# Performance work log

Hardware: AMD Instinct MI355X
Metric: run time of the kernel (lower is better)

The kernel has to match this reference:

```python
import jax, jax.numpy as jnp
import numpy as np

N, D, H = 4096, 128, 8


def setup_inputs() -> dict:
    key = jax.random.key(0)
    ks = jax.random.split(key, 9)
    s = 1.0 / np.sqrt(D)
    return {
        "x": jax.random.normal(ks[0], (N, D), jnp.float32),
        "Wq": jax.random.normal(ks[1], (H, D, D), jnp.float32) * s,
        "bq": jax.random.normal(ks[2], (H, D), jnp.float32) * s,
        "Wk": jax.random.normal(ks[3], (H, D, D), jnp.float32) * s,
        "bk": jax.random.normal(ks[4], (H, D), jnp.float32) * s,
        "Wv": jax.random.normal(ks[5], (H, D, D), jnp.float32) * s,
        "bv": jax.random.normal(ks[6], (H, D), jnp.float32) * s,
        "Wo": jax.random.normal(ks[7], (H * D, D), jnp.float32) * s,
        "bo": jax.random.normal(ks[8], (D,), jnp.float32) * s,
    }


def reference(x, Wq, bq, Wk, bk, Wv, bv, Wo, bo):
    # Batched per-head projections: [H, N, D]
    q = jnp.einsum('nd,hde->hne', x, Wq) + bq[:, None, :]
    k = jnp.einsum('nd,hde->hne', x, Wk) + bk[:, None, :]
    v = jnp.einsum('nd,hde->hne', x, Wv) + bv[:, None, :]
    # Non-standard attention: scores = v @ q.T  -> [H, N, N]
    scores = jnp.einsum('hnd,hmd->hnm', v, q)
    wts = jax.nn.softmax(scores, axis=-1)
    out = jnp.einsum('hnm,hmd->hnd', wts, k)  # [H, N, D]
    # Concat heads along feature dim (head-major order, as torch.cat)
    outs = out.transpose(1, 0, 2).reshape(N, H * D)
    return outs @ Wo + bo
```

## Files before the change

### kernel.cpp

```cpp
#include <hip/hip_runtime.h>
#include <hip/hip_bf16.h>


typedef __attribute__((ext_vector_type(8))) short short8;
typedef __attribute__((ext_vector_type(4))) float f32x4;

#define MFMA(a,b,c) __builtin_amdgcn_mfma_f32_16x16x32_bf16((a),(b),(c),0,0,0)
#define LOG2E 1.44269504088896340736f
#define DEFER_THR 8.0f

#define AS1 __attribute__((address_space(1)))
#define AS3 __attribute__((address_space(3)))
static __device__ __forceinline__ void gld16(const void* g, void* l) {
  __builtin_amdgcn_global_load_lds((const AS1 void*)g, (AS3 void*)l, 16, 0, 0);
}

static __device__ __forceinline__ unsigned short f2bf(float f) {
  union { float f; unsigned u; } v; v.f = f;
  unsigned r = v.u + 0x7fffu + ((v.u >> 16) & 1u);
  return (unsigned short)(r >> 16);
}
static __device__ __forceinline__ float bf2f(unsigned short h) {
  union { unsigned u; float f; } v; v.u = ((unsigned)h) << 16; return v.f;
}
static __device__ __forceinline__ void split2(float f, unsigned short& hi, unsigned short& lo) {
  hi = f2bf(f);
  lo = f2bf(f - bf2f(hi));
}

__global__ __launch_bounds__(256) void kxbf(const float* __restrict__ x,
                                            unsigned short* __restrict__ xh,
                                            unsigned short* __restrict__ xl) {
  int i = blockIdx.x * 256 + threadIdx.x;
  float4 v = reinterpret_cast<const float4*>(x)[i];
  ushort4 oh, ol;
  split2(v.x, oh.x, ol.x); split2(v.y, oh.y, ol.y);
  split2(v.z, oh.z, ol.z); split2(v.w, oh.w, ol.w);
  reinterpret_cast<ushort4*>(xh)[i] = oh;
  reinterpret_cast<ushort4*>(xl)[i] = ol;
}

__global__ __launch_bounds__(256) void kwt(const float* __restrict__ Wq,
                                           const float* __restrict__ Wk,
                                           const float* __restrict__ Wv,
                                           const float* __restrict__ Wo,
                                           unsigned short* __restrict__ WTh,
                                           unsigned short* __restrict__ WTl,
                                           unsigned short* __restrict__ WoT) {
  __shared__ float lds[64 * 130];
  int b = blockIdx.x, t = threadIdx.x;
  const float* src; int isWo;
  if (b < 24) {
    int slot = b >> 3, hh = b & 7;
    src = (slot == 0 ? Wq : (slot == 1 ? Wk : Wv)) + hh * 16384;
    isWo = 0;
  } else {
    src = Wo + (b - 24) * 16384;
    isWo = 1;
  }
  for (int half = 0; half < 2; ++half) {
#pragma unroll
    for (int i = 0; i < 8; ++i) {
      int lin = i * 1024 + t * 4;
      int row = lin >> 7, col = lin & 127;
      float4 v = *reinterpret_cast<const float4*>(src + half * 8192 + lin);
      lds[row * 130 + col + 0] = v.x;
      lds[row * 130 + col + 1] = v.y;
      lds[row * 130 + col + 2] = v.z;
      lds[row * 130 + col + 3] = v.w;
    }
    __syncthreads();
    int e = t >> 1, k0 = (t & 1) * 32;
    float buf[32];
#pragma unroll
    for (int j = 0; j < 32; ++j) buf[j] = lds[(k0 + j) * 130 + e];
    int kg = half * 64 + k0;
    if (!isWo) {
      unsigned short* dh = WTh + b * 16384 + e * 128 + kg;
      unsigned short* dl = WTl + b * 16384 + e * 128 + kg;
#pragma unroll
      for (int c = 0; c < 4; ++c) {
        short8 oh, ol;
#pragma unroll
        for (int jj = 0; jj < 8; ++jj) {
          unsigned short h, l; split2(buf[c * 8 + jj], h, l);
          oh[jj] = (short)h; ol[jj] = (short)l;
        }
        *reinterpret_cast<short8*>(dh + c * 8) = oh;
        *reinterpret_cast<short8*>(dl + c * 8) = ol;
      }
    } else {
      unsigned short* dst = WoT + e * 1024 + (b - 24) * 128 + kg;
#pragma unroll
      for (int c = 0; c < 4; ++c) {
        short8 o;
#pragma unroll
        for (int jj = 0; jj < 8; ++jj) o[jj] = (short)f2bf(buf[c * 8 + jj]);
        *reinterpret_cast<short8*>(dst + c * 8) = o;
      }
    }
    __syncthreads();
  }
}

__global__ __launch_bounds__(256) void kproj(const unsigned short* __restrict__ xh,
                                             const unsigned short* __restrict__ xl,
                                             const unsigned short* __restrict__ WThg,
                                             const unsigned short* __restrict__ WTlg,
                                             const float* __restrict__ bq,
                                             const float* __restrict__ bk,
                                             const float* __restrict__ bv,
                                             unsigned short* __restrict__ Qh,
                                             unsigned short* __restrict__ Vh,
                                             unsigned short* __restrict__ Vl,
                                             unsigned short* __restrict__ Kt) {
  __shared__ __align__(16) unsigned char lds[64 * 128 * 2];
  int nb = blockIdx.x, h = blockIdx.y, z = blockIdx.z;
  int t = threadIdx.x, lane = t & 63, w = t >> 6;
  int r = lane & 15, g = lane >> 4;
  int slot = (z == 0) ? 0 : (z == 1 ? 2 : 1);
  const unsigned short* Wth = WThg + (slot * 8 + h) * 16384;
  const unsigned short* Wtl = WTlg + (slot * 8 + h) * 16384;
  const float* bias = (z == 0) ? bq : (z == 1 ? bv : bk);
  int rowbase = nb * 64 + w * 16;

  short8 ah[4], al[4];
#pragma unroll
  for (int kc = 0; kc < 4; ++kc) {
    ah[kc] = *reinterpret_cast<const short8*>(xh + (rowbase + r) * 128 + kc * 32 + g * 8);
    al[kc] = *reinterpret_cast<const short8*>(xl + (rowbase + r) * 128 + kc * 32 + g * 8);
  }
  f32x4 acc[8];
#pragma unroll
  for (int ct = 0; ct < 8; ++ct) acc[ct] = (f32x4){0.f, 0.f, 0.f, 0.f};
  if (z < 2) {
#pragma unroll
    for (int ct = 0; ct < 8; ++ct) {
#pragma unroll
      for (int kc = 0; kc < 4; ++kc) {
        short8 bh = *reinterpret_cast<const short8*>(Wth + (ct * 16 + r) * 128 + kc * 32 + g * 8);
        short8 bl = *reinterpret_cast<const short8*>(Wtl + (ct * 16 + r) * 128 + kc * 32 + g * 8);
        acc[ct] = MFMA(ah[kc], bh, acc[ct]);
        acc[ct] = MFMA(ah[kc], bl, acc[ct]);
        acc[ct] = MFMA(al[kc], bh, acc[ct]);
      }
    }
    unsigned short* dh = ((z == 0) ? Qh : Vh) + (size_t)h * 4096 * 128;
    unsigned short* dl = Vl + (size_t)h * 4096 * 128;
#pragma unroll
    for (int ct = 0; ct < 8; ++ct) {
      int e = ct * 16 + r;
      float bb = bias[h * 128 + e];
#pragma unroll
      for (int rr = 0; rr < 4; ++rr) {
        int n = rowbase + g * 4 + rr;
        float fv = acc[ct][rr] + bb;
        if (z == 0) {
          dh[n * 128 + e] = f2bf(fv);
        } else {
          unsigned short hi_, lo_; split2(fv, hi_, lo_);
          dh[n * 128 + e] = hi_;
          dl[n * 128 + e] = lo_;
        }
      }
    }
  } else {
#pragma unroll
    for (int ct = 0; ct < 8; ++ct) {
#pragma unroll
      for (int kc = 0; kc < 4; ++kc) {
        short8 bh = *reinterpret_cast<const short8*>(Wth + (ct * 16 + r) * 128 + kc * 32 + g * 8);
        acc[ct] = MFMA(ah[kc], bh, acc[ct]);
      }
    }
#pragma unroll
    for (int ct = 0; ct < 8; ++ct) {
      int e = ct * 16 + r;
      float bb = bias[h * 128 + e];
#pragma unroll
      for (int rr = 0; rr < 4; ++rr) {
        int n = w * 16 + g * 4 + rr;
        unsigned off = ((unsigned)(n * 128 + e) * 2u) ^ ((unsigned)(n & 7) << 4);
        *reinterpret_cast<unsigned short*>(lds + off) = f2bf(acc[ct][rr] + bb);
      }
    }
    __syncthreads();
    int e = t >> 1, n0 = (t & 1) * 32;
    unsigned short buf[32];
#pragma unroll
    for (int j = 0; j < 32; ++j) {
      int n = n0 + j;
      unsigned off = ((unsigned)(n * 128 + e) * 2u) ^ ((unsigned)(n & 7) << 4);
      buf[j] = *reinterpret_cast<unsigned short*>(lds + off);
    }
    unsigned short* dst = Kt + ((size_t)h * 128 + e) * 4096 + nb * 64 + n0;
#pragma unroll
    for (int c = 0; c < 4; ++c) {
      short8 o;
#pragma unroll
      for (int jj = 0; jj < 8; ++jj) o[jj] = (short)buf[c * 8 + jj];
      *reinterpret_cast<short8*>(dst + c * 8) = o;
    }
  }
}

__global__ __launch_bounds__(256, 4) void kattn(
    const unsigned short* __restrict__ Qg,
    const unsigned short* __restrict__ Kt,
    const unsigned short* __restrict__ Vh,
    const unsigned short* __restrict__ Vl,
    unsigned short* __restrict__ Opart,
    float2* __restrict__ ml) {
  __shared__ __align__(16) unsigned char qlds[2][8192];
  __shared__ __align__(16) unsigned char klds[2][8192];
  __shared__ __align__(16) unsigned short plds[4][16 * 40];
  const int h = blockIdx.x, nb = blockIdx.y, z = blockIdx.z;
  const int t = threadIdx.x, lane = t & 63, w = t >> 6;
  const int r = lane & 15, g = lane >> 4;
  const unsigned char* Qb = (const unsigned char*)(Qg + (size_t)h * 4096 * 128);
  const unsigned char* Kb = (const unsigned char*)(Kt + (size_t)h * 128 * 4096);

  const int qrow = t >> 4;
  const unsigned qcb = (unsigned)((t & 15) * 16);
  const int krow = t >> 2;
  const unsigned kmb = (unsigned)((t & 3) * 16);

  const int vrow = nb * 64 + w * 16 + r;
  short8 vah[4], val[4];
#pragma unroll
  for (int kc = 0; kc < 4; ++kc) {
    vah[kc] = *reinterpret_cast<const short8*>(Vh + (size_t)h * 4096 * 128 + (size_t)vrow * 128 + kc * 32 + g * 8);
    val[kc] = *reinterpret_cast<const short8*>(Vl + (size_t)h * 4096 * 128 + (size_t)vrow * 128 + kc * 32 + g * 8);
  }

  f32x4 oacc[8];
#pragma unroll
  for (int dt = 0; dt < 8; ++dt) oacc[dt] = (f32x4){0.f, 0.f, 0.f, 0.f};
  float mrun = -3e38f, lrun = 0.f;
  const int mt0 = z * 64;

#define STAGE(buf, mtile) do {                                                   \
    const size_t mQ = (size_t)(mtile) * 32 * 256;                                \
    const size_t mK = (size_t)(mtile) * 32 * 2;                                  \
    _Pragma("unroll")                                                            \
    for (int j = 0; j < 2; ++j) {                                                \
      int row = qrow + j * 16;                                                   \
      gld16(Qb + mQ + (size_t)row * 256 + (qcb ^ ((unsigned)(row & 7) << 4)),    \
            &qlds[buf][j * 4096 + t * 16]);                                      \
    }                                                                            \
    _Pragma("unroll")                                                            \
    for (int j = 0; j < 2; ++j) {                                                \
      int d = krow + j * 64;                                                     \
      gld16(Kb + (size_t)d * 8192 + mK + kmb,                                    \
            &klds[buf][j * 4096 + t * 16]);                                      \
    }                                                                            \
  } while (0)

  STAGE(0, mt0);
  __syncthreads();

  const unsigned qsw = ((unsigned)(r & 7)) << 4;
  for (int it = 0; it < 64; ++it) {
    const int buf = it & 1;
    if (it < 63) STAGE(buf ^ 1, mt0 + it + 1);
    f32x4 s0 = (f32x4){0.f, 0.f, 0.f, 0.f};
    f32x4 s1 = (f32x4){0.f, 0.f, 0.f, 0.f};
    __builtin_amdgcn_s_setprio(1);
#pragma unroll
    for (int kc = 0; kc < 4; ++kc) {
      unsigned col = (unsigned)(kc * 64 + g * 16);
      short8 q0 = *reinterpret_cast<const short8*>(&qlds[buf][(unsigned)r * 256 + (col ^ qsw)]);
      short8 q1 = *reinterpret_cast<const short8*>(&qlds[buf][(unsigned)(16 + r) * 256 + (col ^ qsw)]);
      s0 = MFMA(q0, vah[kc], s0);
      s1 = MFMA(q1, vah[kc], s1);
      s0 = MFMA(q0, val[kc], s0);
      s1 = MFMA(q1, val[kc], s1);
    }
    __builtin_amdgcn_s_setprio(0);
    float mx = fmaxf(fmaxf(fmaxf(s0[0], s0[1]), fmaxf(s0[2], s0[3])),
                     fmaxf(fmaxf(s1[0], s1[1]), fmaxf(s1[2], s1[3])));
    mx = fmaxf(mx, __shfl_xor(mx, 16));
    mx = fmaxf(mx, __shfl_xor(mx, 32));
    if (__any(mx > mrun + DEFER_THR)) {
      float nm = fmaxf(mrun, mx);
      float sc = exp2f((mrun - nm) * LOG2E);
      lrun *= sc;
#pragma unroll
      for (int dt = 0; dt < 8; ++dt) oacc[dt] *= sc;
      mrun = nm;
    }
    float p[8];
#pragma unroll
    for (int j = 0; j < 4; ++j) {
      p[j]     = exp2f((s0[j] - mrun) * LOG2E);
      p[4 + j] = exp2f((s1[j] - mrun) * LOG2E);
    }
    float ps = ((p[0] + p[1]) + (p[2] + p[3])) + ((p[4] + p[5]) + (p[6] + p[7]));
    ps += __shfl_xor(ps, 16);
    ps += __shfl_xor(ps, 32);
    lrun += ps;
    ushort4 pk0, pk1;
    pk0.x = f2bf(p[0]); pk0.y = f2bf(p[1]); pk0.z = f2bf(p[2]); pk0.w = f2bf(p[3]);
    pk1.x = f2bf(p[4]); pk1.y = f2bf(p[5]); pk1.z = f2bf(p[6]); pk1.w = f2bf(p[7]);
    unsigned short* pw = &plds[w][r * 40];
    *reinterpret_cast<ushort4*>(pw + g * 4)      = pk0;
    *reinterpret_cast<ushort4*>(pw + 16 + g * 4) = pk1;
    short8 pa = *reinterpret_cast<const short8*>(&plds[w][r * 40 + g * 8]);
    __builtin_amdgcn_s_setprio(1);
#pragma unroll
    for (int dt = 0; dt < 8; ++dt) {
      short8 kb = *reinterpret_cast<const short8*>(&klds[buf][(unsigned)(dt * 16 + r) * 64 + (unsigned)(g * 16)]);
      oacc[dt] = MFMA(kb, pa, oacc[dt]);
    }
    __builtin_amdgcn_s_setprio(0);
    __syncthreads();
  }
#undef STAGE
  unsigned short* Ob = Opart + ((size_t)(z * 8 + h) * 4096 + vrow) * 128;
#pragma unroll
  for (int dt = 0; dt < 8; ++dt) {
    ushort4 o4;
    o4.x = f2bf(oacc[dt][0]); o4.y = f2bf(oacc[dt][1]);
    o4.z = f2bf(oacc[dt][2]); o4.w = f2bf(oacc[dt][3]);
    *reinterpret_cast<ushort4*>(Ob + dt * 16 + g * 4) = o4;
  }
  if (g == 0) ml[(size_t)(z * 8 + h) * 4096 + vrow] = make_float2(mrun, lrun);
}

__global__ __launch_bounds__(256) void kmerge(const unsigned short* __restrict__ Opart,
                                              const float2* __restrict__ ml,
                                              unsigned short* __restrict__ OUTS) {
  int tid = blockIdx.x * 256 + threadIdx.x;
  int q = tid & 31, n = (tid >> 5) & 4095, h = tid >> 17;
  float2 ml0 = ml[(size_t)h * 4096 + n];
  float2 ml1 = ml[(size_t)(8 + h) * 4096 + n];
  float M = fmaxf(ml0.x, ml1.x);
  float a0 = exp2f((ml0.x - M) * LOG2E);
  float a1 = exp2f((ml1.x - M) * LOG2E);
  float inv = 1.0f / (ml0.y * a0 + ml1.y * a1);
  a0 *= inv; a1 *= inv;
  ushort4 o0 = *reinterpret_cast<const ushort4*>(Opart + ((size_t)h * 4096 + n) * 128 + q * 4);
  ushort4 o1 = *reinterpret_cast<const ushort4*>(Opart + ((size_t)(8 + h) * 4096 + n) * 128 + q * 4);
  ushort4 o;
  o.x = f2bf(bf2f(o0.x) * a0 + bf2f(o1.x) * a1);
  o.y = f2bf(bf2f(o0.y) * a0 + bf2f(o1.y) * a1);
  o.z = f2bf(bf2f(o0.z) * a0 + bf2f(o1.z) * a1);
  o.w = f2bf(bf2f(o0.w) * a0 + bf2f(o1.w) * a1);
  *reinterpret_cast<ushort4*>(OUTS + (size_t)n * 1024 + h * 128 + q * 4) = o;
}

__global__ __launch_bounds__(256) void kout(const unsigned short* __restrict__ OUTS,
                                            const unsigned short* __restrict__ WoT,
                                            const float* __restrict__ bo,
                                            float* __restrict__ out) {
  int rb = blockIdx.x, ch = blockIdx.y;
  int t = threadIdx.x, lane = t & 63, w = t >> 6;
  int r = lane & 15, g = lane >> 4;
  int row = rb * 16 + r;
  int e0 = ch * 64 + w * 16;
  f32x4 acc = (f32x4){0.f, 0.f, 0.f, 0.f};
#pragma unroll
  for (int kc = 0; kc < 32; ++kc) {
    short8 a = *reinterpret_cast<const short8*>(OUTS + (size_t)row * 1024 + kc * 32 + g * 8);
    short8 b = *reinterpret_cast<const short8*>(WoT + (size_t)(e0 + r) * 1024 + kc * 32 + g * 8);
    acc = MFMA(a, b, acc);
  }
  float bov = bo[e0 + r];
#pragma unroll
  for (int rr = 0; rr < 4; ++rr) {
    int n = rb * 16 + g * 4 + rr;
    out[(size_t)n * 128 + e0 + r] = acc[rr] + bov;
  }
}

extern "C" void kernel_launch(void* const* d_in, const int* in_sizes, int n_in,
                              void* d_out, int out_size, void* d_ws, size_t ws_size,
                              hipStream_t stream) {
  const float* x  = (const float*)d_in[0];
  const float* Wq = (const float*)d_in[1];
  const float* bq = (const float*)d_in[2];
  const float* Wk = (const float*)d_in[3];
  const float* bk = (const float*)d_in[4];
  const float* Wv = (const float*)d_in[5];
  const float* bv = (const float*)d_in[6];
  const float* Wo = (const float*)d_in[7];
  const float* bo = (const float*)d_in[8];
  float* out = (float*)d_out;

  unsigned short* ws = (unsigned short*)d_ws;
  unsigned short* xh    = ws;
  unsigned short* xl    = xh + 524288;
  unsigned short* WTh   = xl + 524288;
  unsigned short* WTl   = WTh + 393216;
  unsigned short* WoT   = WTl + 393216;
  unsigned short* Qh    = WoT + 131072;
  unsigned short* Vh    = Qh + 4194304;
  unsigned short* Vl    = Vh + 4194304;
  unsigned short* Kt    = Vl + 4194304;
  unsigned short* OUTS  = Kt + 4194304;
  unsigned short* Opart = OUTS + 4194304;
  float2*         mlp   = (float2*)(Opart + 8388608);

  kxbf<<<512, 256, 0, stream>>>(x, xh, xl);
  kwt<<<32, 256, 0, stream>>>(Wq, Wk, Wv, Wo, WTh, WTl, WoT);
  kproj<<<dim3(64, 8, 3), 256, 0, stream>>>(xh, xl, WTh, WTl, bq, bk, bv,
                                            Qh, Vh, Vl, Kt);
  kattn<<<dim3(8, 64, 2), 256, 0, stream>>>(Qh, Kt, Vh, Vl, Opart, mlp);
  kmerge<<<4096, 256, 0, stream>>>(Opart, mlp, OUTS);
  kout<<<dim3(256, 2), 256, 0, stream>>>(OUTS, WoT, bo, out);
}
```

Before: 285.4 us.

## Fuse x conversion into projection, widen attention tiles, fuse merge into output GEMM

Drops the separate x bf16-split kernel and splits x inside the projection kernel, which now computes Q, V and K in one block per row tile instead of three z-slices. The attention kernel moves to 128-thread blocks in which each wave handles 32 V rows, so every staged Q/K tile is reused across twice as many rows. The split-softmax merge is folded into the output projection, which also computes all 128 output columns per block. This removes two launches and the OUTS intermediate, at the cost of more registers in the attention kernel and scalar (non-vector) Opart stores.

After: 275.4 us. 3.5% less time.

```diff
diff --git a/kernel.cpp b/kernel.cpp
--- a/kernel.cpp
+++ b/kernel.cpp
@@ -26,18 +26,6 @@
 static __device__ __forceinline__ void split2(float f, unsigned short& hi, unsigned short& lo) {
   hi = f2bf(f);
   lo = f2bf(f - bf2f(hi));
-}
-
-__global__ __launch_bounds__(256) void kxbf(const float* __restrict__ x,
-                                            unsigned short* __restrict__ xh,
-                                            unsigned short* __restrict__ xl) {
-  int i = blockIdx.x * 256 + threadIdx.x;
-  float4 v = reinterpret_cast<const float4*>(x)[i];
-  ushort4 oh, ol;
-  split2(v.x, oh.x, ol.x); split2(v.y, oh.y, ol.y);
-  split2(v.z, oh.z, ol.z); split2(v.w, oh.w, ol.w);
-  reinterpret_cast<ushort4*>(xh)[i] = oh;
-  reinterpret_cast<ushort4*>(xl)[i] = ol;
 }
 
 __global__ __launch_bounds__(256) void kwt(const float* __restrict__ Wq,
@@ -103,37 +91,45 @@
   }
 }
 
-__global__ __launch_bounds__(256) void kproj(const unsigned short* __restrict__ xh,
-                                             const unsigned short* __restrict__ xl,
-                                             const unsigned short* __restrict__ WThg,
-                                             const unsigned short* __restrict__ WTlg,
-                                             const float* __restrict__ bq,
-                                             const float* __restrict__ bk,
-                                             const float* __restrict__ bv,
-                                             unsigned short* __restrict__ Qh,
-                                             unsigned short* __restrict__ Vh,
-                                             unsigned short* __restrict__ Vl,
-                                             unsigned short* __restrict__ Kt) {
+__global__ __launch_bounds__(256) void kprojf(const float* __restrict__ x,
+                                              const unsigned short* __restrict__ WThg,
+                                              const unsigned short* __restrict__ WTlg,
+                                              const float* __restrict__ bq,
+                                              const float* __restrict__ bk,
+                                              const float* __restrict__ bv,
+                                              unsigned short* __restrict__ Qh,
+                                              unsigned short* __restrict__ Vh,
+                                              unsigned short* __restrict__ Vl,
+                                              unsigned short* __restrict__ Kt) {
   __shared__ __align__(16) unsigned char lds[64 * 128 * 2];
-  int nb = blockIdx.x, h = blockIdx.y, z = blockIdx.z;
+  int nb = blockIdx.x, h = blockIdx.y;
   int t = threadIdx.x, lane = t & 63, w = t >> 6;
   int r = lane & 15, g = lane >> 4;
-  int slot = (z == 0) ? 0 : (z == 1 ? 2 : 1);
-  const unsigned short* Wth = WThg + (slot * 8 + h) * 16384;
-  const unsigned short* Wtl = WTlg + (slot * 8 + h) * 16384;
-  const float* bias = (z == 0) ? bq : (z == 1 ? bv : bk);
   int rowbase = nb * 64 + w * 16;
 
   short8 ah[4], al[4];
 #pragma unroll
   for (int kc = 0; kc < 4; ++kc) {
-    ah[kc] = *reinterpret_cast<const short8*>(xh + (rowbase + r) * 128 + kc * 32 + g * 8);
-    al[kc] = *reinterpret_cast<const short8*>(xl + (rowbase + r) * 128 + kc * 32 + g * 8);
-  }
+    const float* xp = x + (size_t)(rowbase + r) * 128 + kc * 32 + g * 8;
+    float4 f0 = *reinterpret_cast<const float4*>(xp);
+    float4 f1 = *reinterpret_cast<const float4*>(xp + 4);
+    unsigned short hi_, lo_;
+    split2(f0.x, hi_, lo_); ah[kc][0] = (short)hi_; al[kc][0] = (short)lo_;
+    split2(f0.y, hi_, lo_); ah[kc][1] = (short)hi_; al[kc][1] = (short)lo_;
+    split2(f0.z, hi_, lo_); ah[kc][2] = (short)hi_; al[kc][2] = (short)lo_;
+    split2(f0.w, hi_, lo_); ah[kc][3] = (short)hi_; al[kc][3] = (short)lo_;
+    split2(f1.x, hi_, lo_); ah[kc][4] = (short)hi_; al[kc][4] = (short)lo_;
+    split2(f1.y, hi_, lo_); ah[kc][5] = (short)hi_; al[kc][5] = (short)lo_;
+    split2(f1.z, hi_, lo_); ah[kc][6] = (short)hi_; al[kc][6] = (short)lo_;
+    split2(f1.w, hi_, lo_); ah[kc][7] = (short)hi_; al[kc][7] = (short)lo_;
+  }
+
   f32x4 acc[8];
-#pragma unroll
-  for (int ct = 0; ct < 8; ++ct) acc[ct] = (f32x4){0.f, 0.f, 0.f, 0.f};
-  if (z < 2) {
+  {
+    const unsigned short* Wth = WThg + (0 * 8 + h) * 16384;
+    const unsigned short* Wtl = WTlg + (0 * 8 + h) * 16384;
+#pragma unroll
+    for (int ct = 0; ct < 8; ++ct) acc[ct] = (f32x4){0.f, 0.f, 0.f, 0.f};
 #pragma unroll
     for (int ct = 0; ct < 8; ++ct) {
 #pragma unroll
@@ -145,26 +141,53 @@
         acc[ct] = MFMA(al[kc], bh, acc[ct]);
       }
     }
-    unsigned short* dh = ((z == 0) ? Qh : Vh) + (size_t)h * 4096 * 128;
-    unsigned short* dl = Vl + (size_t)h * 4096 * 128;
+    unsigned short* dh = Qh + (size_t)h * 4096 * 128;
 #pragma unroll
     for (int ct = 0; ct < 8; ++ct) {
       int e = ct * 16 + r;
-      float bb = bias[h * 128 + e];
+      float bb = bq[h * 128 + e];
 #pragma unroll
       for (int rr = 0; rr < 4; ++rr) {
         int n = rowbase + g * 4 + rr;
-        float fv = acc[ct][rr] + bb;
-        if (z == 0) {
-          dh[n * 128 + e] = f2bf(fv);
-        } else {
-          unsigned short hi_, lo_; split2(fv, hi_, lo_);
-          dh[n * 128 + e] = hi_;
-          dl[n * 128 + e] = lo_;
-        }
-      }
-    }
-  } else {
+        dh[n * 128 + e] = f2bf(acc[ct][rr] + bb);
+      }
+    }
+  }
+  {
+    const unsigned short* Wth = WThg + (2 * 8 + h) * 16384;
+    const unsigned short* Wtl = WTlg + (2 * 8 + h) * 16384;
+#pragma unroll
+    for (int ct = 0; ct < 8; ++ct) acc[ct] = (f32x4){0.f, 0.f, 0.f, 0.f};
+#pragma unroll
+    for (int ct = 0; ct < 8; ++ct) {
+#pragma unroll
+      for (int kc = 0; kc < 4; ++kc) {
+        short8 bh = *reinterpret_cast<const short8*>(Wth + (ct * 16 + r) * 128 + kc * 32 + g * 8);
+        short8 bl = *reinterpret_cast<const short8*>(Wtl + (ct * 16 + r) * 128 + kc * 32 + g * 8);
+        acc[ct] = MFMA(ah[kc], bh, acc[ct]);
+        acc[ct] = MFMA(ah[kc], bl, acc[ct]);
+        acc[ct] = MFMA(al[kc], bh, acc[ct]);
+      }
+    }
+    unsigned short* dh = Vh + (size_t)h * 4096 * 128;
+    unsigned short* dl = Vl + (size_t)h * 4096 * 128;
+#pragma unroll
+    for (int ct = 0; ct < 8; ++ct) {
+      int e = ct * 16 + r;
+      float bb = bv[h * 128 + e];
+#pragma unroll
+      for (int rr = 0; rr < 4; ++rr) {
+        int n = rowbase + g * 4 + rr;
+        unsigned short hi_, lo_; split2(acc[ct][rr] + bb, hi_, lo_);
+        dh[n * 128 + e] = hi_;
+        dl[n * 128 + e] = lo_;
+      }
+    }
+  }
+  {
+    const unsigned short* Wth = WThg + (1 * 8 + h) * 16384;
+#pragma unroll
+    for (int ct = 0; ct < 8; ++ct) acc[ct] = (f32x4){0.f, 0.f, 0.f, 0.f};
 #pragma unroll
     for (int ct = 0; ct < 8; ++ct) {
 #pragma unroll
@@ -176,7 +199,7 @@
 #pragma unroll
     for (int ct = 0; ct < 8; ++ct) {
       int e = ct * 16 + r;
-      float bb = bias[h * 128 + e];
+      float bb = bk[h * 128 + e];
 #pragma unroll
       for (int rr = 0; rr < 4; ++rr) {
         int n = w * 16 + g * 4 + rr;
@@ -204,7 +227,7 @@
   }
 }
 
-__global__ __launch_bounds__(256, 4) void kattn(
+__global__ __launch_bounds__(128, 2) void kattn(
     const unsigned short* __restrict__ Qg,
     const unsigned short* __restrict__ Kt,
     const unsigned short* __restrict__ Vh,
@@ -213,46 +236,48 @@
     float2* __restrict__ ml) {
   __shared__ __align__(16) unsigned char qlds[2][8192];
   __shared__ __align__(16) unsigned char klds[2][8192];
-  __shared__ __align__(16) unsigned short plds[4][16 * 40];
+  __shared__ __align__(16) unsigned short plds[2][32 * 40];
   const int h = blockIdx.x, nb = blockIdx.y, z = blockIdx.z;
   const int t = threadIdx.x, lane = t & 63, w = t >> 6;
   const int r = lane & 15, g = lane >> 4;
   const unsigned char* Qb = (const unsigned char*)(Qg + (size_t)h * 4096 * 128);
   const unsigned char* Kb = (const unsigned char*)(Kt + (size_t)h * 128 * 4096);
 
-  const int qrow = t >> 4;
-  const unsigned qcb = (unsigned)((t & 15) * 16);
-  const int krow = t >> 2;
-  const unsigned kmb = (unsigned)((t & 3) * 16);
-
-  const int vrow = nb * 64 + w * 16 + r;
-  short8 vah[4], val[4];
+  const int vbase = nb * 64 + w * 32;
+  short8 va0h[4], va0l[4], va1h[4], va1l[4];
 #pragma unroll
   for (int kc = 0; kc < 4; ++kc) {
-    vah[kc] = *reinterpret_cast<const short8*>(Vh + (size_t)h * 4096 * 128 + (size_t)vrow * 128 + kc * 32 + g * 8);
-    val[kc] = *reinterpret_cast<const short8*>(Vl + (size_t)h * 4096 * 128 + (size_t)vrow * 128 + kc * 32 + g * 8);
-  }
-
-  f32x4 oacc[8];
-#pragma unroll
-  for (int dt = 0; dt < 8; ++dt) oacc[dt] = (f32x4){0.f, 0.f, 0.f, 0.f};
-  float mrun = -3e38f, lrun = 0.f;
+    size_t o0 = (size_t)h * 4096 * 128 + (size_t)(vbase + r) * 128 + kc * 32 + g * 8;
+    size_t o1 = (size_t)h * 4096 * 128 + (size_t)(vbase + 16 + r) * 128 + kc * 32 + g * 8;
+    va0h[kc] = *reinterpret_cast<const short8*>(Vh + o0);
+    va0l[kc] = *reinterpret_cast<const short8*>(Vl + o0);
+    va1h[kc] = *reinterpret_cast<const short8*>(Vh + o1);
+    va1l[kc] = *reinterpret_cast<const short8*>(Vl + o1);
+  }
+
+  f32x4 oacc0[8], oacc1[8];
+#pragma unroll
+  for (int dt = 0; dt < 8; ++dt) {
+    oacc0[dt] = (f32x4){0.f, 0.f, 0.f, 0.f};
+    oacc1[dt] = (f32x4){0.f, 0.f, 0.f, 0.f};
+  }
+  float m0run = -3e38f, l0run = 0.f, m1run = -3e38f, l1run = 0.f;
   const int mt0 = z * 64;
 
 #define STAGE(buf, mtile) do {                                                   \
-    const size_t mQ = (size_t)(mtile) * 32 * 256;                                \
-    const size_t mK = (size_t)(mtile) * 32 * 2;                                  \
+    const unsigned char* qsrc = Qb + (size_t)(mtile) * 8192;                     \
+    const unsigned char* ksrc = Kb + (size_t)(mtile) * 64;                       \
     _Pragma("unroll")                                                            \
-    for (int j = 0; j < 2; ++j) {                                                \
-      int row = qrow + j * 16;                                                   \
-      gld16(Qb + mQ + (size_t)row * 256 + (qcb ^ ((unsigned)(row & 7) << 4)),    \
-            &qlds[buf][j * 4096 + t * 16]);                                      \
+    for (int j = 0; j < 4; ++j) {                                                \
+      int row = j * 8 + (t >> 4);                                                \
+      gld16(qsrc + (size_t)row * 256 + (((unsigned)(t & 15) * 16) ^ ((unsigned)(row & 7) << 4)), \
+            &qlds[buf][j * 2048 + t * 16]);                                      \
     }                                                                            \
     _Pragma("unroll")                                                            \
-    for (int j = 0; j < 2; ++j) {                                                \
-      int d = krow + j * 64;                                                     \
-      gld16(Kb + (size_t)d * 8192 + mK + kmb,                                    \
-            &klds[buf][j * 4096 + t * 16]);                                      \
+    for (int j = 0; j < 4; ++j) {                                                \
+      int row = j * 32 + (t >> 2);                                               \
+      gld16(ksrc + (size_t)row * 8192 + (unsigned)(t & 3) * 16,                  \
+            &klds[buf][j * 2048 + t * 16]);                                      \
     }                                                                            \
   } while (0)
 
@@ -263,113 +288,144 @@
   for (int it = 0; it < 64; ++it) {
     const int buf = it & 1;
     if (it < 63) STAGE(buf ^ 1, mt0 + it + 1);
-    f32x4 s0 = (f32x4){0.f, 0.f, 0.f, 0.f};
-    f32x4 s1 = (f32x4){0.f, 0.f, 0.f, 0.f};
+    f32x4 s00 = (f32x4){0.f, 0.f, 0.f, 0.f};
+    f32x4 s10 = (f32x4){0.f, 0.f, 0.f, 0.f};
+    f32x4 s01 = (f32x4){0.f, 0.f, 0.f, 0.f};
+    f32x4 s11 = (f32x4){0.f, 0.f, 0.f, 0.f};
     __builtin_amdgcn_s_setprio(1);
 #pragma unroll
     for (int kc = 0; kc < 4; ++kc) {
       unsigned col = (unsigned)(kc * 64 + g * 16);
       short8 q0 = *reinterpret_cast<const short8*>(&qlds[buf][(unsigned)r * 256 + (col ^ qsw)]);
       short8 q1 = *reinterpret_cast<const short8*>(&qlds[buf][(unsigned)(16 + r) * 256 + (col ^ qsw)]);
-      s0 = MFMA(q0, vah[kc], s0);
-      s1 = MFMA(q1, vah[kc], s1);
-      s0 = MFMA(q0, val[kc], s0);
-      s1 = MFMA(q1, val[kc], s1);
+      s00 = MFMA(q0, va0h[kc], s00);
+      s10 = MFMA(q1, va0h[kc], s10);
+      s01 = MFMA(q0, va1h[kc], s01);
+      s11 = MFMA(q1, va1h[kc], s11);
+      s00 = MFMA(q0, va0l[kc], s00);
+      s10 = MFMA(q1, va0l[kc], s10);
+      s01 = MFMA(q0, va1l[kc], s01);
+      s11 = MFMA(q1, va1l[kc], s11);
     }
     __builtin_amdgcn_s_setprio(0);
-    float mx = fmaxf(fmaxf(fmaxf(s0[0], s0[1]), fmaxf(s0[2], s0[3])),
-                     fmaxf(fmaxf(s1[0], s1[1]), fmaxf(s1[2], s1[3])));
-    mx = fmaxf(mx, __shfl_xor(mx, 16));
-    mx = fmaxf(mx, __shfl_xor(mx, 32));
-    if (__any(mx > mrun + DEFER_THR)) {
-      float nm = fmaxf(mrun, mx);
-      float sc = exp2f((mrun - nm) * LOG2E);
-      lrun *= sc;
-#pragma unroll
-      for (int dt = 0; dt < 8; ++dt) oacc[dt] *= sc;
-      mrun = nm;
-    }
-    float p[8];
+    float mx0 = fmaxf(fmaxf(fmaxf(s00[0], s00[1]), fmaxf(s00[2], s00[3])),
+                      fmaxf(fmaxf(s10[0], s10[1]), fmaxf(s10[2], s10[3])));
+    float mx1 = fmaxf(fmaxf(fmaxf(s01[0], s01[1]), fmaxf(s01[2], s01[3])),
+                      fmaxf(fmaxf(s11[0], s11[1]), fmaxf(s11[2], s11[3])));
+    mx0 = fmaxf(mx0, __shfl_xor(mx0, 16)); mx0 = fmaxf(mx0, __shfl_xor(mx0, 32));
+    mx1 = fmaxf(mx1, __shfl_xor(mx1, 16)); mx1 = fmaxf(mx1, __shfl_xor(mx1, 32));
+    if (__any(mx0 > m0run + DEFER_THR)) {
+      float nm = fmaxf(m0run, mx0);
+      float sc = exp2f((m0run - nm) * LOG2E);
+      l0run *= sc;
+#pragma unroll
+      for (int dt = 0; dt < 8; ++dt) oacc0[dt] *= sc;
+      m0run = nm;
+    }
+    if (__any(mx1 > m1run + DEFER_THR)) {
+      float nm = fmaxf(m1run, mx1);
+      float sc = exp2f((m1run - nm) * LOG2E);
+      l1run *= sc;
+#pragma unroll
+      for (int dt = 0; dt < 8; ++dt) oacc1[dt] *= sc;
+      m1run = nm;
+    }
+    float p0[8], p1[8];
 #pragma unroll
     for (int j = 0; j < 4; ++j) {
-      p[j]     = exp2f((s0[j] - mrun) * LOG2E);
-      p[4 + j] = exp2f((s1[j] - mrun) * LOG2E);
-    }
-    float ps = ((p[0] + p[1]) + (p[2] + p[3])) + ((p[4] + p[5]) + (p[6] + p[7]));
-    ps += __shfl_xor(ps, 16);
-    ps += __shfl_xor(ps, 32);
-    lrun += ps;
-    ushort4 pk0, pk1;
-    pk0.x = f2bf(p[0]); pk0.y = f2bf(p[1]); pk0.z = f2bf(p[2]); pk0.w = f2bf(p[3]);
-    pk1.x = f2bf(p[4]); pk1.y = f2bf(p[5]); pk1.z = f2bf(p[6]); pk1.w = f2bf(p[7]);
-    unsigned short* pw = &plds[w][r * 40];
-    *reinterpret_cast<ushort4*>(pw + g * 4)      = pk0;
-    *reinterpret_cast<ushort4*>(pw + 16 + g * 4) = pk1;
-    short8 pa = *reinterpret_cast<const short8*>(&plds[w][r * 40 + g * 8]);
+      p0[j]     = exp2f((s00[j] - m0run) * LOG2E);
+      p0[4 + j] = exp2f((s10[j] - m0run) * LOG2E);
+      p1[j]     = exp2f((s01[j] - m1run) * LOG2E);
+      p1[4 + j] = exp2f((s11[j] - m1run) * LOG2E);
+    }
+    float ps0 = ((p0[0] + p0[1]) + (p0[2] + p0[3])) + ((p0[4] + p0[5]) + (p0[6] + p0[7]));
+    float ps1 = ((p1[0] + p1[1]) + (p1[2] + p1[3])) + ((p1[4] + p1[5]) + (p1[6] + p1[7]));
+    ps0 += __shfl_xor(ps0, 16); ps0 += __shfl_xor(ps0, 32);
+    ps1 += __shfl_xor(ps1, 16); ps1 += __shfl_xor(ps1, 32);
+    l0run += ps0;
+    l1run += ps1;
+    {
+      ushort4 a, b, c, d;
+      a.x = f2bf(p0[0]); a.y = f2bf(p0[1]); a.z = f2bf(p0[2]); a.w = f2bf(p0[3]);
+      b.x = f2bf(p0[4]); b.y = f2bf(p0[5]); b.z = f2bf(p0[6]); b.w = f2bf(p0[7]);
+      c.x = f2bf(p1[0]); c.y = f2bf(p1[1]); c.z = f2bf(p1[2]); c.w = f2bf(p1[3]);
+      d.x = f2bf(p1[4]); d.y = f2bf(p1[5]); d.z = f2bf(p1[6]); d.w = f2bf(p1[7]);
+      unsigned short* pw = &plds[w][0];
+      *reinterpret_cast<ushort4*>(pw + r * 40 + g * 4)             = a;
+      *reinterpret_cast<ushort4*>(pw + r * 40 + 16 + g * 4)        = b;
+      *reinterpret_cast<ushort4*>(pw + (16 + r) * 40 + g * 4)      = c;
+      *reinterpret_cast<ushort4*>(pw + (16 + r) * 40 + 16 + g * 4) = d;
+    }
+    short8 pa0 = *reinterpret_cast<const short8*>(&plds[w][r * 40 + g * 8]);
+    short8 pa1 = *reinterpret_cast<const short8*>(&plds[w][(16 + r) * 40 + g * 8]);
     __builtin_amdgcn_s_setprio(1);
 #pragma unroll
     for (int dt = 0; dt < 8; ++dt) {
       short8 kb = *reinterpret_cast<const short8*>(&klds[buf][(unsigned)(dt * 16 + r) * 64 + (unsigned)(g * 16)]);
-      oacc[dt] = MFMA(kb, pa, oacc[dt]);
+      oacc0[dt] = MFMA(kb, pa0, oacc0[dt]);
+      oacc1[dt] = MFMA(kb, pa1, oacc1[dt]);
     }
     __builtin_amdgcn_s_setprio(0);
     __syncthreads();
   }
 #undef STAGE
-  unsigned short* Ob = Opart + ((size_t)(z * 8 + h) * 4096 + vrow) * 128;
+  unsigned short* Ob = Opart + (size_t)(z * 8 + h) * 4096 * 128;
 #pragma unroll
   for (int dt = 0; dt < 8; ++dt) {
-    ushort4 o4;
-    o4.x = f2bf(oacc[dt][0]); o4.y = f2bf(oacc[dt][1]);
-    o4.z = f2bf(oacc[dt][2]); o4.w = f2bf(oacc[dt][3]);
-    *reinterpret_cast<ushort4*>(Ob + dt * 16 + g * 4) = o4;
-  }
-  if (g == 0) ml[(size_t)(z * 8 + h) * 4096 + vrow] = make_float2(mrun, lrun);
-}
-
-__global__ __launch_bounds__(256) void kmerge(const unsigned short* __restrict__ Opart,
-                                              const float2* __restrict__ ml,
-                                              unsigned short* __restrict__ OUTS) {
-  int tid = blockIdx.x * 256 + threadIdx.x;
-  int q = tid & 31, n = (tid >> 5) & 4095, h = tid >> 17;
-  float2 ml0 = ml[(size_t)h * 4096 + n];
-  float2 ml1 = ml[(size_t)(8 + h) * 4096 + n];
-  float M = fmaxf(ml0.x, ml1.x);
-  float a0 = exp2f((ml0.x - M) * LOG2E);
-  float a1 = exp2f((ml1.x - M) * LOG2E);
-  float inv = 1.0f / (ml0.y * a0 + ml1.y * a1);
-  a0 *= inv; a1 *= inv;
-  ushort4 o0 = *reinterpret_cast<const ushort4*>(Opart + ((size_t)h * 4096 + n) * 128 + q * 4);
-  ushort4 o1 = *reinterpret_cast<const ushort4*>(Opart + ((size_t)(8 + h) * 4096 + n) * 128 + q * 4);
-  ushort4 o;
-  o.x = f2bf(bf2f(o0.x) * a0 + bf2f(o1.x) * a1);
-  o.y = f2bf(bf2f(o0.y) * a0 + bf2f(o1.y) * a1);
-  o.z = f2bf(bf2f(o0.z) * a0 + bf2f(o1.z) * a1);
-  o.w = f2bf(bf2f(o0.w) * a0 + bf2f(o1.w) * a1);
-  *reinterpret_cast<ushort4*>(OUTS + (size_t)n * 1024 + h * 128 + q * 4) = o;
-}
-
-__global__ __launch_bounds__(256) void kout(const unsigned short* __restrict__ OUTS,
-                                            const unsigned short* __restrict__ WoT,
-                                            const float* __restrict__ bo,
-                                            float* __restrict__ out) {
-  int rb = blockIdx.x, ch = blockIdx.y;
+#pragma unroll
+    for (int rr = 0; rr < 4; ++rr) {
+      int d = dt * 16 + g * 4 + rr;
+      Ob[(size_t)(vbase + r) * 128 + d]      = f2bf(oacc0[dt][rr]);
+      Ob[(size_t)(vbase + 16 + r) * 128 + d] = f2bf(oacc1[dt][rr]);
+    }
+  }
+  if (g == 0) ml[(size_t)(z * 8 + h) * 4096 + vbase + r]      = make_float2(m0run, l0run);
+  if (g == 1) ml[(size_t)(z * 8 + h) * 4096 + vbase + 16 + r] = make_float2(m1run, l1run);
+}
+
+__global__ __launch_bounds__(256) void koutm(const unsigned short* __restrict__ Opart,
+                                             const float2* __restrict__ ml,
+                                             const unsigned short* __restrict__ WoT,
+                                             const float* __restrict__ bo,
+                                             float* __restrict__ out) {
+  int rb = blockIdx.x;
   int t = threadIdx.x, lane = t & 63, w = t >> 6;
   int r = lane & 15, g = lane >> 4;
   int row = rb * 16 + r;
-  int e0 = ch * 64 + w * 16;
-  f32x4 acc = (f32x4){0.f, 0.f, 0.f, 0.f};
+  float a0[8], a1[8];
+#pragma unroll
+  for (int h = 0; h < 8; ++h) {
+    float2 m0 = ml[(size_t)h * 4096 + row];
+    float2 m1 = ml[(size_t)(8 + h) * 4096 + row];
+    float M = fmaxf(m0.x, m1.x);
+    float e0 = exp2f((m0.x - M) * LOG2E);
+    float e1 = exp2f((m1.x - M) * LOG2E);
+    float inv = 1.0f / (m0.y * e0 + m1.y * e1);
+    a0[h] = e0 * inv; a1[h] = e1 * inv;
+  }
+  f32x4 acc0 = (f32x4){0.f, 0.f, 0.f, 0.f};
+  f32x4 acc1 = (f32x4){0.f, 0.f, 0.f, 0.f};
 #pragma unroll
   for (int kc = 0; kc < 32; ++kc) {
-    short8 a = *reinterpret_cast<const short8*>(OUTS + (size_t)row * 1024 + kc * 32 + g * 8);
-    short8 b = *reinterpret_cast<const short8*>(WoT + (size_t)(e0 + r) * 1024 + kc * 32 + g * 8);
-    acc = MFMA(a, b, acc);
-  }
-  float bov = bo[e0 + r];
+    int h = kc >> 2;
+    int dof = (kc & 3) * 32 + g * 8;
+    short8 o0 = *reinterpret_cast<const short8*>(Opart + ((size_t)h * 4096 + row) * 128 + dof);
+    short8 o1 = *reinterpret_cast<const short8*>(Opart + ((size_t)(8 + h) * 4096 + row) * 128 + dof);
+    short8 af;
+#pragma unroll
+    for (int j = 0; j < 8; ++j)
+      af[j] = (short)f2bf(bf2f((unsigned short)o0[j]) * a0[h] +
+                          bf2f((unsigned short)o1[j]) * a1[h]);
+    short8 b0 = *reinterpret_cast<const short8*>(WoT + (size_t)(w * 32 + r) * 1024 + kc * 32 + g * 8);
+    short8 b1 = *reinterpret_cast<const short8*>(WoT + (size_t)(w * 32 + 16 + r) * 1024 + kc * 32 + g * 8);
+    acc0 = MFMA(af, b0, acc0);
+    acc1 = MFMA(af, b1, acc1);
+  }
 #pragma unroll
   for (int rr = 0; rr < 4; ++rr) {
     int n = rb * 16 + g * 4 + rr;
-    out[(size_t)n * 128 + e0 + r] = acc[rr] + bov;
+    out[(size_t)n * 128 + w * 32 + r]      = acc0[rr] + bo[w * 32 + r];
+    out[(size_t)n * 128 + w * 32 + 16 + r] = acc1[rr] + bo[w * 32 + 16 + r];
   }
 }
 
@@ -388,24 +444,18 @@
   float* out = (float*)d_out;
 
   unsigned short* ws = (unsigned short*)d_ws;
-  unsigned short* xh    = ws;
-  unsigned short* xl    = xh + 524288;
-  unsigned short* WTh   = xl + 524288;
+  unsigned short* WTh   = ws;
   unsigned short* WTl   = WTh + 393216;
   unsigned short* WoT   = WTl + 393216;
   unsigned short* Qh    = WoT + 131072;
   unsigned short* Vh    = Qh + 4194304;
   unsigned short* Vl    = Vh + 4194304;
   unsigned short* Kt    = Vl + 4194304;
-  unsigned short* OUTS  = Kt + 4194304;
-  unsigned short* Opart = OUTS + 4194304;
+  unsigned short* Opart = Kt + 4194304;
   float2*         mlp   = (float2*)(Opart + 8388608);
 
-  kxbf<<<512, 256, 0, stream>>>(x, xh, xl);
   kwt<<<32, 256, 0, stream>>>(Wq, Wk, Wv, Wo, WTh, WTl, WoT);
-  kproj<<<dim3(64, 8, 3), 256, 0, stream>>>(xh, xl, WTh, WTl, bq, bk, bv,
-                                            Qh, Vh, Vl, Kt);
-  kattn<<<dim3(8, 64, 2), 256, 0, stream>>>(Qh, Kt, Vh, Vl, Opart, mlp);
-  kmerge<<<4096, 256, 0, stream>>>(Opart, mlp, OUTS);
-  kout<<<dim3(256, 2), 256, 0, stream>>>(OUTS, WoT, bo, out);
-}
+  kprojf<<<dim3(64, 8), 256, 0, stream>>>(x, WTh, WTl, bq, bk, bv, Qh, Vh, Vl, Kt);
+  kattn<<<dim3(8, 64, 2), 128, 0, stream>>>(Qh, Kt, Vh, Vl, Opart, mlp);
+  koutm<<<256, 256, 0, stream>>>(Opart, mlp, WoT, bo, out);
+}
```
